# Kernel tuning notes

Measured on AMD Instinct MI355X. Metric: run time of the kernel, lower is better.

The kernel has to match this reference:

```python
import jax, jax.numpy as jnp
import numpy as np

B, NFRAME, NPATCH = 4, 16, 64
SEQ = NFRAME * NPATCH          # 1024
DIM, DEPTH, HEADS, DHEAD, MLP = 768, 6, 12, 64, 3072
INNER = HEADS * DHEAD          # 768
SCALE = DHEAD ** -0.5
EPS = 1e-5


def setup_inputs() -> dict:
    key = jax.random.key(0)
    ks = jax.random.split(key, 16)
    w = lambda k, shape, s=0.02: (jax.random.normal(k, shape, dtype=jnp.float32) * s)
    return {
        "x": jax.random.normal(ks[0], (B, SEQ, DIM), dtype=jnp.float32),
        "pos": w(ks[1], (1, SEQ, DIM), 1.0),
        "ln1_w": jnp.ones((DEPTH, DIM), jnp.float32),
        "ln1_b": jnp.zeros((DEPTH, DIM), jnp.float32),
        "wqkv": w(ks[2], (DEPTH, DIM, 3 * INNER)),
        "wo": w(ks[3], (DEPTH, INNER, DIM)),
        "bo": jnp.zeros((DEPTH, DIM), jnp.float32),
        "ln2_w": jnp.ones((DEPTH, DIM), jnp.float32),
        "ln2_b": jnp.zeros((DEPTH, DIM), jnp.float32),
        "w1": w(ks[4], (DEPTH, DIM, MLP)),
        "b1": jnp.zeros((DEPTH, MLP), jnp.float32),
        "w2": w(ks[5], (DEPTH, MLP, DIM)),
        "b2": jnp.zeros((DEPTH, DIM), jnp.float32),
        "lnf_w": jnp.ones((DIM,), jnp.float32),
        "lnf_b": jnp.zeros((DIM,), jnp.float32),
    }


def _ln(x, w, b):
    mu = jnp.mean(x, axis=-1, keepdims=True)
    var = jnp.mean(jnp.square(x - mu), axis=-1, keepdims=True)
    return (x - mu) * jax.lax.rsqrt(var + EPS) * w + b


def _forward(x, pos, ln1_w, ln1_b, wqkv, wo, bo, ln2_w, ln2_b, w1, b1, w2, b2, lnf_w, lnf_b):
    n = x.shape[1]
    x = x + pos[:, :n]
    # block-causal mask: token in frame i attends to all tokens in frames 0..i
    frames = jnp.arange(n) // NPATCH
    mask = frames[:, None] >= frames[None, :]            # [S, S] bool
    neg = jnp.finfo(x.dtype).min

    def layer(x, p):
        l1w, l1b, Wqkv, Wo, Bo, l2w, l2b, W1, B1, W2, B2 = p
        h = _ln(x, l1w, l1b)
        qkv = h @ Wqkv                                   # [B,S,3*inner]
        q, k, v = jnp.split(qkv, 3, axis=-1)
        rs = lambda t: t.reshape(x.shape[0], n, HEADS, DHEAD).transpose(0, 2, 1, 3)
        q, k, v = rs(q), rs(k), rs(v)                    # [B,H,S,D]
        scores = jnp.einsum("bhqd,bhkd->bhqk", q, k) * SCALE
        scores = jnp.where(mask, scores, neg)
        attn = jax.nn.softmax(scores, axis=-1)
        out = jnp.einsum("bhqk,bhkd->bhqd", attn, v)
        out = out.transpose(0, 2, 1, 3).reshape(x.shape[0], n, INNER)
        x = x + out @ Wo + Bo
        h = _ln(x, l2w, l2b)
        h = jax.nn.gelu(h @ W1 + B1, approximate=False) @ W2 + B2
        x = x + h
        return x, None

    params = (ln1_w, ln1_b, wqkv, wo, bo, ln2_w, ln2_b, w1, b1, w2, b2)
    x, _ = jax.lax.scan(layer, x, params)
    return _ln(x, lnf_w, lnf_b)


def reference(x, pos, ln1_w, ln1_b, wqkv, wo, bo, ln2_w, ln2_b, w1, b1, w2, b2, lnf_w, lnf_b):
    return _forward(x, pos, ln1_w, ln1_b, wqkv, wo, bo, ln2_w, ln2_b, w1, b1, w2, b2, lnf_w, lnf_b)
```

## Files before the change

### kernel.cpp

```cpp
#include <hip/hip_runtime.h>
#include <cmath>

#define SCALE 0.125f

using f32x4  = __attribute__((ext_vector_type(4))) float;
using bf16x8 = __attribute__((ext_vector_type(8))) short;

#define S_WAITCNT_VMCNT(N) asm volatile("s_waitcnt vmcnt(" #N ")" ::: "memory")

__device__ __forceinline__ short f2bf(float f) {
  union { float f; unsigned u; } x; x.f = f;
  return (short)((x.u + 0x7fffu + ((x.u >> 16) & 1u)) >> 16);
}

__device__ __forceinline__ unsigned cvt_pk_bf16(float lo, float hi) {
  unsigned r;
  asm volatile("v_cvt_pk_bf16_f32 %0, %1, %2" : "=v"(r) : "v"(lo), "v"(hi));
  return r;
}

__device__ __forceinline__ void gl_lds16(const void* g, void* l) {
  __builtin_amdgcn_global_load_lds(
      (const __attribute__((address_space(1))) void*)(uintptr_t)g,
      (__attribute__((address_space(3))) void*)(uintptr_t)l,
      16, 0, 0);
}

__global__ __launch_bounds__(256) void wtrans_k(const float* __restrict__ src,
                                                short* __restrict__ dst,
                                                int K, int N)
{
  __shared__ float tile[32][33];
  const size_t base = (size_t)blockIdx.z * K * N;
  const int n0 = blockIdx.x * 32, k0 = blockIdx.y * 32;
  const int tx = threadIdx.x, ty = threadIdx.y;
#pragma unroll
  for (int i = 0; i < 4; ++i)
    tile[ty + 8*i][tx] = src[base + (size_t)(k0 + ty + 8*i)*N + n0 + tx];
  __syncthreads();
#pragma unroll
  for (int i = 0; i < 4; ++i)
    dst[base + (size_t)(n0 + ty + 8*i)*K + k0 + tx] = f2bf(tile[tx][ty + 8*i]);
}

template<int OUT_F32, int FUSE0>
__global__ __launch_bounds__(256)
void ln_k(const float* __restrict__ x, const float* __restrict__ pos,
          const float* __restrict__ w, const float* __restrict__ bb,
          void* __restrict__ out, float* __restrict__ xout)
{
  const int row  = blockIdx.x*4 + (threadIdx.x >> 6);
  const int lane = threadIdx.x & 63;
  const float* xr = x + (size_t)row*768;
  float4 v[3];
  float s = 0.f, s2 = 0.f;
#pragma unroll
  for (int i = 0; i < 3; ++i) {
    const int c = i*256 + lane*4;
    v[i] = *(const float4*)(xr + c);
    if constexpr (FUSE0) {
      const float4 p = *(const float4*)(pos + (size_t)(row & 1023)*768 + c);
      v[i].x += p.x; v[i].y += p.y; v[i].z += p.z; v[i].w += p.w;
      *(float4*)(xout + (size_t)row*768 + c) = v[i];
    }
    s  += v[i].x + v[i].y + v[i].z + v[i].w;
    s2 += v[i].x*v[i].x + v[i].y*v[i].y + v[i].z*v[i].z + v[i].w*v[i].w;
  }
#pragma unroll
  for (int off = 1; off < 64; off <<= 1) {
    s  += __shfl_xor(s,  off);
    s2 += __shfl_xor(s2, off);
  }
  const float mu  = s * (1.0f/768.0f);
  const float inv = rsqrtf(s2*(1.0f/768.0f) - mu*mu + 1e-5f);
#pragma unroll
  for (int i = 0; i < 3; ++i) {
    const int c = i*256 + lane*4;
    const float4 wv = *(const float4*)(w  + c);
    const float4 bv = *(const float4*)(bb + c);
    const float o0 = (v[i].x - mu)*inv*wv.x + bv.x;
    const float o1 = (v[i].y - mu)*inv*wv.y + bv.y;
    const float o2 = (v[i].z - mu)*inv*wv.z + bv.z;
    const float o3 = (v[i].w - mu)*inv*wv.w + bv.w;
    if constexpr (OUT_F32) {
      float4 ov; ov.x=o0; ov.y=o1; ov.z=o2; ov.w=o3;
      *(float4*)((float*)out + (size_t)row*768 + c) = ov;
    } else {
      short4 ov; ov.x=f2bf(o0); ov.y=f2bf(o1); ov.z=f2bf(o2); ov.w=f2bf(o3);
      *(short4*)((short*)out + (size_t)row*768 + c) = ov;
    }
  }
}

template<int EPI, int BN, int KS = 1, int DB = 0>
__global__ __launch_bounds__(256, 2)
void gemm_bt(const short* __restrict__ A, const short* __restrict__ Bt,
             int M, int N, int K,
             short* __restrict__ outB, float* __restrict__ xio,
             const float* __restrict__ bias, short* __restrict__ vt)
{
  constexpr int NI = BN / 32;
  constexpr int NB = DB ? 2 : 1;
  __shared__ __align__(16) short As[NB][128][64];
  __shared__ __align__(16) short Bs[NB][BN][64];
  const int t    = threadIdx.x;
  const int lane = t & 63;
  const int g    = lane >> 4, r15 = lane & 15;
  const int w    = t >> 6;
  const int wm   = w >> 1, wn = w & 1;
  const int nx  = gridDim.x;
  const int bid = blockIdx.y*nx + blockIdx.x;
  const int cpx = (nx * gridDim.y) >> 3;
  const int nb  = (bid & 7)*cpx + (bid >> 3);
  const int row0 = (nb / nx) * 128;
  const int col0 = (nb % nx) * BN;
  const int kz   = (KS > 1) ? blockIdx.z : 0;
  const int kzo  = kz * (K / KS);
  const int srow   = lane >> 3;
  const int schunk = (lane & 7) ^ srow;
  f32x4 acc[4][NI] = {};
  const int nk = (K / KS) >> 6;
  auto stageT = [&](int buf, int kt) {
    const int k0 = kzo + (kt << 6);
#pragma unroll
    for (int i = 0; i < 4; ++i) {
      const int r = w*32 + i*8;
      gl_lds16(A + (size_t)(row0 + r + srow)*K + k0 + schunk*8, &As[buf][r][0]);
    }
#pragma unroll
    for (int i = 0; i < BN/32; ++i) {
      const int r = w*(BN/4) + i*8;
      gl_lds16(Bt + (size_t)(col0 + r + srow)*K + k0 + schunk*8, &Bs[buf][r][0]);
    }
  };
  auto computeT = [&](int buf) {
#pragma unroll
    for (int kk = 0; kk < 2; ++kk) {
      bf16x8 af[4], bfr[NI];
#pragma unroll
      for (int mi = 0; mi < 4; ++mi) {
        const int r = wm*64 + mi*16 + r15;
        const int c = (kk*4 + g) ^ (r & 7);
        af[mi] = *(const bf16x8*)(&As[buf][r][c*8]);
      }
#pragma unroll
      for (int ni = 0; ni < NI; ++ni) {
        const int r = wn*(BN/2) + ni*16 + r15;
        const int c = (kk*4 + g) ^ (r & 7);
        bfr[ni] = *(const bf16x8*)(&Bs[buf][r][c*8]);
      }
#pragma unroll
      for (int mi = 0; mi < 4; ++mi)
#pragma unroll
        for (int ni = 0; ni < NI; ++ni)
          acc[mi][ni] = __builtin_amdgcn_mfma_f32_16x16x32_bf16(af[mi], bfr[ni], acc[mi][ni], 0, 0, 0);
    }
  };
  if constexpr (DB) {
    stageT(0, 0);
    for (int kt = 0; kt < nk; ++kt) {
      const int cur = kt & 1;
      __builtin_amdgcn_sched_barrier(0);
      if (kt + 1 < nk) {
        stageT(cur ^ 1, kt + 1);
        if constexpr (BN == 64) S_WAITCNT_VMCNT(6); else S_WAITCNT_VMCNT(8);
      } else {
        S_WAITCNT_VMCNT(0);
      }
      __builtin_amdgcn_sched_barrier(0);
      __builtin_amdgcn_s_barrier();
      __builtin_amdgcn_sched_barrier(0);
      computeT(cur);
      __builtin_amdgcn_sched_barrier(0);
      __builtin_amdgcn_s_barrier();
    }
  } else {
    for (int kt = 0; kt < nk; ++kt) {
      stageT(0, kt);
      __syncthreads();
      computeT(0);
      __syncthreads();
    }
  }
#pragma unroll
  for (int mi = 0; mi < 4; ++mi)
#pragma unroll
    for (int ni = 0; ni < NI; ++ni) {
      const int rr0 = row0 + wm*64 + mi*16 + g*4;
      const int cc  = col0 + wn*(BN/2) + ni*16 + r15;
#pragma unroll
      for (int reg = 0; reg < 4; ++reg) {
        const float v = acc[mi][ni][reg];
        if constexpr (EPI == 0) {
          outB[(size_t)(rr0 + reg)*N + cc] = f2bf(v);
        } else if constexpr (EPI == 1) {
          const float u = v + bias[cc];
          outB[(size_t)(rr0 + reg)*N + cc] = f2bf(0.5f*u*(1.0f + erff(u*0.70710678f)));
        } else {
          const size_t o = (size_t)(rr0 + reg)*N + cc;
          if constexpr (KS == 1) {
            xio[o] += v + bias[cc];
          } else {
            unsafeAtomicAdd(&xio[o], v + (kz == 0 ? bias[cc] : 0.0f));
          }
        }
      }
      if constexpr (EPI == 0) {
        if (vt != nullptr && cc >= 1536) {
          const int hd = cc - 1536;
          const int bb = rr0 >> 10, s = rr0 & 1023;
          short4 o;
          o.x = f2bf(acc[mi][ni][0]); o.y = f2bf(acc[mi][ni][1]);
          o.z = f2bf(acc[mi][ni][2]); o.w = f2bf(acc[mi][ni][3]);
          *(short4*)(vt + (((size_t)bb*768 + hd) << 10) + s) = o;
        }
      }
    }
}

__global__ __launch_bounds__(256, 2)
void attn_k(const short* __restrict__ qkv, const short* __restrict__ vt,
            short* __restrict__ aout)
{
  const int qf = (blockIdx.x*5 + blockIdx.y) & 15;
  const int h = blockIdx.y, b = blockIdx.z;
  const int t = threadIdx.x, w = t >> 6, lane = t & 63;
  const int g = lane >> 4, r15 = lane & 15;
  __shared__ __align__(16) short Kl[2][64][64];
  __shared__ __align__(16) short Vl[2][64][64];
  __shared__ __align__(16) short P_lds[4][16][72];
  short* Prow = &P_lds[w][r15][0];
  const int tok0 = b*1024 + qf*64 + w*16;
  bf16x8 aq[2];
#pragma unroll
  for (int kk = 0; kk < 2; ++kk)
    aq[kk] = *(const bf16x8*)(qkv + (size_t)(tok0 + r15)*2304 + h*64 + kk*32 + g*8);
  const short* kbase = qkv + (size_t)(b*1024)*2304 + 768 + h*64;
  const short* vbase = vt + (size_t)((b*12 + h)*64)*1024;
  const int lr8 = lane >> 3;
  const int lc  = lane & 7;
  auto stage = [&](int buf, int kf) {
#pragma unroll
    for (int i = 0; i < 2; ++i) {
      const int r0 = w*16 + i*8;
      const int lr = r0 + lr8;
      const int c  = lc ^ (lr & 7);
      gl_lds16(kbase + (size_t)(kf*64 + lr)*2304 + c*8, &Kl[buf][r0][0]);
      gl_lds16(vbase + (size_t)lr*1024 + kf*64 + c*8, &Vl[buf][r0][0]);
    }
  };
  float m = -1e30f, lsum = 0.f;
  f32x4 O[4] = {};
  const int nf = qf + 1;
  stage(0, 0);
  __syncthreads();
  for (int kf = 0; kf < nf; ++kf) {
    const int cur = kf & 1;
    if (kf + 1 < nf) stage(cur ^ 1, kf + 1);
    f32x4 s[4];
    __builtin_amdgcn_s_setprio(1);
#pragma unroll
    for (int nj = 0; nj < 4; ++nj) {
      const int tr = nj*16 + r15;
      const bf16x8 k0 = *(const bf16x8*)(&Kl[cur][tr][((0*4 + g) ^ (tr & 7)) * 8]);
      const bf16x8 k1 = *(const bf16x8*)(&Kl[cur][tr][((1*4 + g) ^ (tr & 7)) * 8]);
      f32x4 z = {};
      z     = __builtin_amdgcn_mfma_f32_16x16x32_bf16(k0, aq[0], z, 0, 0, 0);
      s[nj] = __builtin_amdgcn_mfma_f32_16x16x32_bf16(k1, aq[1], z, 0, 0, 0);
    }
    __builtin_amdgcn_s_setprio(0);
    bf16x8 av[2][4];
#pragma unroll
    for (int kc = 0; kc < 2; ++kc)
#pragma unroll
      for (int di = 0; di < 4; ++di) {
        const int dr = di*16 + r15;
        av[kc][di] = *(const bf16x8*)(&Vl[cur][dr][((kc*4 + g) ^ (dr & 7)) * 8]);
      }
    float pmax = -1e30f;
#pragma unroll
    for (int nj = 0; nj < 4; ++nj)
      pmax = fmaxf(pmax, fmaxf(fmaxf(s[nj][0], s[nj][1]), fmaxf(s[nj][2], s[nj][3])));
    pmax *= SCALE;
    pmax = fmaxf(pmax, __shfl_xor(pmax, 16));
    pmax = fmaxf(pmax, __shfl_xor(pmax, 32));
    if (!__all(pmax - m <= 8.0f)) {
      const float mn = fmaxf(m, pmax);
      const float fac = __expf(m - mn);
      m = mn; lsum *= fac;
#pragma unroll
      for (int di = 0; di < 4; ++di) {
        O[di][0] *= fac; O[di][1] *= fac; O[di][2] *= fac; O[di][3] *= fac;
      }
    }
    float rs = 0.f;
    short4 pw[4];
#pragma unroll
    for (int nj = 0; nj < 4; ++nj) {
      const float p0 = __expf(s[nj][0]*SCALE - m);
      const float p1 = __expf(s[nj][1]*SCALE - m);
      const float p2 = __expf(s[nj][2]*SCALE - m);
      const float p3 = __expf(s[nj][3]*SCALE - m);
      rs += (p0 + p1) + (p2 + p3);
      union { unsigned u; short2 s2; } c0, c1;
      c0.u = cvt_pk_bf16(p0, p1);
      c1.u = cvt_pk_bf16(p2, p3);
      pw[nj].x = c0.s2.x; pw[nj].y = c0.s2.y;
      pw[nj].z = c1.s2.x; pw[nj].w = c1.s2.y;
    }
    rs += __shfl_xor(rs, 16);
    rs += __shfl_xor(rs, 32);
    lsum += rs;
#pragma unroll
    for (int nj = 0; nj < 4; ++nj)
      *(short4*)(Prow + nj*16 + g*4) = pw[nj];
    asm volatile("s_waitcnt lgkmcnt(0)" ::: "memory");
    __builtin_amdgcn_sched_barrier(0);
    __builtin_amdgcn_s_setprio(1);
#pragma unroll
    for (int kc = 0; kc < 2; ++kc) {
      const bf16x8 bp = *(const bf16x8*)(Prow + kc*32 + g*8);
#pragma unroll
      for (int di = 0; di < 4; ++di)
        O[di] = __builtin_amdgcn_mfma_f32_16x16x32_bf16(av[kc][di], bp, O[di], 0, 0, 0);
    }
    __builtin_amdgcn_s_setprio(0);
    __syncthreads();
  }
  const float invl = 1.0f / lsum;
#pragma unroll
  for (int di = 0; di < 4; ++di) {
    uint2 uv;
    uv.x = cvt_pk_bf16(O[di][0]*invl, O[di][1]*invl);
    uv.y = cvt_pk_bf16(O[di][2]*invl, O[di][3]*invl);
    *(uint2*)(aout + (size_t)(tok0 + r15)*768 + h*64 + di*16 + g*4) = uv;
  }
}

extern "C" void kernel_launch(void* const* d_in, const int* in_sizes, int n_in,
                              void* d_out, int out_size, void* d_ws, size_t ws_size,
                              hipStream_t stream)
{
  (void)in_sizes; (void)n_in; (void)out_size; (void)ws_size;
  const float* x_in = (const float*)d_in[0];
  const float* pos  = (const float*)d_in[1];
  const float* ln1w = (const float*)d_in[2];
  const float* ln1b = (const float*)d_in[3];
  const float* wqkv = (const float*)d_in[4];
  const float* wo   = (const float*)d_in[5];
  const float* bo   = (const float*)d_in[6];
  const float* ln2w = (const float*)d_in[7];
  const float* ln2b = (const float*)d_in[8];
  const float* w1   = (const float*)d_in[9];
  const float* b1   = (const float*)d_in[10];
  const float* w2   = (const float*)d_in[11];
  const float* b2   = (const float*)d_in[12];
  const float* lnfw = (const float*)d_in[13];
  const float* lnfb = (const float*)d_in[14];

  size_t off = 0;
  auto carve = [&](size_t bytes) {
    void* p = (char*)d_ws + off;
    off += (bytes + 255) & ~(size_t)255;
    return p;
  };
  short* wqkvT = (short*)carve((size_t)6*2304*768*2);
  short* woT   = (short*)carve((size_t)6*768*768*2);
  short* w1T   = (short*)carve((size_t)6*3072*768*2);
  short* w2T   = (short*)carve((size_t)6*768*3072*2);
  float* x     = (float*)carve((size_t)4096*768*4);
  short* hbuf  = (short*)carve((size_t)4096*768*2);
  short* qkv   = (short*)carve((size_t)4096*2304*2);
  short* vt    = (short*)carve((size_t)48*64*1024*2);
  short* aout  = (short*)carve((size_t)4096*768*2);
  short* mid   = (short*)carve((size_t)4096*3072*2);

  wtrans_k<<<dim3(72,24,6), dim3(32,8), 0, stream>>>(wqkv, wqkvT, 768, 2304);
  wtrans_k<<<dim3(24,24,6), dim3(32,8), 0, stream>>>(wo,   woT,   768, 768);
  wtrans_k<<<dim3(96,24,6), dim3(32,8), 0, stream>>>(w1,   w1T,   768, 3072);
  wtrans_k<<<dim3(24,96,6), dim3(32,8), 0, stream>>>(w2,   w2T,   3072, 768);

  for (int L = 0; L < 6; ++L) {
    if (L == 0)
      ln_k<0,1><<<1024, 256, 0, stream>>>(x_in, pos, ln1w, ln1b, hbuf, x);
    else
      ln_k<0,0><<<1024, 256, 0, stream>>>(x, nullptr, ln1w + L*768, ln1b + L*768, hbuf, nullptr);
    gemm_bt<0,128,1,0><<<dim3(18,32), 256, 0, stream>>>(hbuf, wqkvT + (size_t)L*2304*768,
                                                        4096, 2304, 768, qkv, nullptr, nullptr, vt);
    attn_k<<<dim3(16,12,4), 256, 0, stream>>>(qkv, vt, aout);
    gemm_bt<2,64,2,1><<<dim3(12,32,2), 256, 0, stream>>>(aout, woT + (size_t)L*768*768,
                                                         4096, 768, 768, nullptr, x, bo + L*768, nullptr);
    ln_k<0,0><<<1024, 256, 0, stream>>>(x, nullptr, ln2w + L*768, ln2b + L*768, hbuf, nullptr);
    gemm_bt<1,128,1,0><<<dim3(24,32), 256, 0, stream>>>(hbuf, w1T + (size_t)L*3072*768,
                                                        4096, 3072, 768, mid, nullptr, b1 + L*3072, nullptr);
    gemm_bt<2,64,4,1><<<dim3(12,32,4), 256, 0, stream>>>(mid, w2T + (size_t)L*768*3072,
                                                         4096, 768, 3072, nullptr, x, b2 + L*768, nullptr);
  }
  ln_k<1,0><<<1024, 256, 0, stream>>>(x, nullptr, lnfw, lnfb, d_out, nullptr);
}
```

Baseline: 1.054 ms.

## Load GEMM B operand directly to registers for output-projection GEMMs

Adds a BREG variant of the double-buffered GEMM where each wave loads its B fragments from global memory straight into registers, one k-step ahead, instead of staging them through LDS. Only the A tile is still staged in shared memory. The Wo and W2 projections use this path, and the W2 split-K factor drops from 4 to 2. This cuts LDS traffic and the LDS footprint but raises register pressure, and the B loads read strided rows that are not coalesced; fewer split-K blocks also means less parallelism for the W2 GEMM and fewer atomic/accumulate passes.

Result: slower. 1.102 ms (+4.5%).

```diff
diff --git a/kernel.cpp b/kernel.cpp
--- a/kernel.cpp
+++ b/kernel.cpp
@@ -92,7 +92,7 @@
   }
 }
 
-template<int EPI, int BN, int KS = 1, int DB = 0>
+template<int EPI, int BN, int KS = 1, int DB = 0, int BREG = 0>
 __global__ __launch_bounds__(256, 2)
 void gemm_bt(const short* __restrict__ A, const short* __restrict__ Bt,
              int M, int N, int K,
@@ -101,8 +101,9 @@
 {
   constexpr int NI = BN / 32;
   constexpr int NB = DB ? 2 : 1;
+  constexpr int NBB = BREG ? 1 : NB;
   __shared__ __align__(16) short As[NB][128][64];
-  __shared__ __align__(16) short Bs[NB][BN][64];
+  __shared__ __align__(16) short Bs[NBB][BN][64];
   const int t    = threadIdx.x;
   const int lane = t & 63;
   const int g    = lane >> 4, r15 = lane & 15;
@@ -120,13 +121,16 @@
   const int schunk = (lane & 7) ^ srow;
   f32x4 acc[4][NI] = {};
   const int nk = (K / KS) >> 6;
-  auto stageT = [&](int buf, int kt) {
+  auto stageA = [&](int buf, int kt) {
     const int k0 = kzo + (kt << 6);
 #pragma unroll
     for (int i = 0; i < 4; ++i) {
       const int r = w*32 + i*8;
       gl_lds16(A + (size_t)(row0 + r + srow)*K + k0 + schunk*8, &As[buf][r][0]);
     }
+  };
+  auto stageB = [&](int buf, int kt) {
+    const int k0 = kzo + (kt << 6);
 #pragma unroll
     for (int i = 0; i < BN/32; ++i) {
       const int r = w*(BN/4) + i*8;
@@ -156,13 +160,69 @@
           acc[mi][ni] = __builtin_amdgcn_mfma_f32_16x16x32_bf16(af[mi], bfr[ni], acc[mi][ni], 0, 0, 0);
     }
   };
-  if constexpr (DB) {
-    stageT(0, 0);
+  if constexpr (DB && BREG) {
+    bf16x8 b0[2][2], b1[2][2];
+    auto loadB = [&](int kt, bf16x8 (&bx)[2][2]) {
+      const int k0 = kzo + (kt << 6);
+#pragma unroll
+      for (int kk = 0; kk < 2; ++kk)
+#pragma unroll
+        for (int ni = 0; ni < 2; ++ni)
+          bx[kk][ni] = *(const bf16x8*)(Bt + (size_t)(col0 + wn*32 + ni*16 + r15)*K
+                                        + k0 + kk*32 + g*8);
+    };
+    auto computeR = [&](int buf, bf16x8 (&bx)[2][2]) {
+#pragma unroll
+      for (int kk = 0; kk < 2; ++kk) {
+        bf16x8 af[4];
+#pragma unroll
+        for (int mi = 0; mi < 4; ++mi) {
+          const int r = wm*64 + mi*16 + r15;
+          const int c = (kk*4 + g) ^ (r & 7);
+          af[mi] = *(const bf16x8*)(&As[buf][r][c*8]);
+        }
+#pragma unroll
+        for (int mi = 0; mi < 4; ++mi)
+#pragma unroll
+          for (int ni = 0; ni < 2; ++ni)
+            acc[mi][ni] = __builtin_amdgcn_mfma_f32_16x16x32_bf16(af[mi], bx[kk][ni], acc[mi][ni], 0, 0, 0);
+      }
+    };
+    loadB(0, b0);
+    stageA(0, 0);
+    for (int kt = 0; kt < nk; kt += 2) {
+      __builtin_amdgcn_sched_barrier(0);
+      loadB(kt + 1, b1);
+      stageA(1, kt + 1);
+      S_WAITCNT_VMCNT(8);
+      __builtin_amdgcn_sched_barrier(0);
+      __builtin_amdgcn_s_barrier();
+      __builtin_amdgcn_sched_barrier(0);
+      computeR(0, b0);
+      __builtin_amdgcn_sched_barrier(0);
+      __builtin_amdgcn_s_barrier();
+      __builtin_amdgcn_sched_barrier(0);
+      loadB(kt + 2 < nk ? kt + 2 : 0, b0);
+      if (kt + 2 < nk) {
+        stageA(0, kt + 2);
+        S_WAITCNT_VMCNT(8);
+      } else {
+        S_WAITCNT_VMCNT(4);
+      }
+      __builtin_amdgcn_sched_barrier(0);
+      __builtin_amdgcn_s_barrier();
+      __builtin_amdgcn_sched_barrier(0);
+      computeR(1, b1);
+      __builtin_amdgcn_sched_barrier(0);
+      __builtin_amdgcn_s_barrier();
+    }
+  } else if constexpr (DB) {
+    stageA(0, 0); stageB(0, 0);
     for (int kt = 0; kt < nk; ++kt) {
       const int cur = kt & 1;
       __builtin_amdgcn_sched_barrier(0);
       if (kt + 1 < nk) {
-        stageT(cur ^ 1, kt + 1);
+        stageA(cur ^ 1, kt + 1); stageB(cur ^ 1, kt + 1);
         if constexpr (BN == 64) S_WAITCNT_VMCNT(6); else S_WAITCNT_VMCNT(8);
       } else {
         S_WAITCNT_VMCNT(0);
@@ -176,7 +236,7 @@
     }
   } else {
     for (int kt = 0; kt < nk; ++kt) {
-      stageT(0, kt);
+      stageA(0, kt); stageB(0, kt);
       __syncthreads();
       computeT(0);
       __syncthreads();
@@ -388,13 +448,13 @@
     gemm_bt<0,128,1,0><<<dim3(18,32), 256, 0, stream>>>(hbuf, wqkvT + (size_t)L*2304*768,
                                                         4096, 2304, 768, qkv, nullptr, nullptr, vt);
     attn_k<<<dim3(16,12,4), 256, 0, stream>>>(qkv, vt, aout);
-    gemm_bt<2,64,2,1><<<dim3(12,32,2), 256, 0, stream>>>(aout, woT + (size_t)L*768*768,
-                                                         4096, 768, 768, nullptr, x, bo + L*768, nullptr);
+    gemm_bt<2,64,2,1,1><<<dim3(12,32,2), 256, 0, stream>>>(aout, woT + (size_t)L*768*768,
+                                                           4096, 768, 768, nullptr, x, bo + L*768, nullptr);
     ln_k<0,0><<<1024, 256, 0, stream>>>(x, nullptr, ln2w + L*768, ln2b + L*768, hbuf, nullptr);
     gemm_bt<1,128,1,0><<<dim3(24,32), 256, 0, stream>>>(hbuf, w1T + (size_t)L*3072*768,
                                                         4096, 3072, 768, mid, nullptr, b1 + L*3072, nullptr);
-    gemm_bt<2,64,4,1><<<dim3(12,32,4), 256, 0, stream>>>(mid, w2T + (size_t)L*768*3072,
-                                                         4096, 768, 3072, nullptr, x, b2 + L*768, nullptr);
+    gemm_bt<2,64,2,1,1><<<dim3(12,32,2), 256, 0, stream>>>(mid, w2T + (size_t)L*768*3072,
+                                                           4096, 768, 3072, nullptr, x, b2 + L*768, nullptr);
   }
   ln_k<1,0><<<1024, 256, 0, stream>>>(x, nullptr, lnfw, lnfb, d_out, nullptr);
 }
```
